# Kernel optimization log

Hardware: AMD Instinct MI355X
Metric: run time of the kernel (lower is better)

Reference implementation:

```python
import jax, jax.numpy as jnp
import numpy as np

N_RAYS = 131072
N_SAMPLES = 64
N_IMPORTANCE = 128
NEAR, FAR = 2.0, 6.0


def setup_inputs() -> dict:
    key = jax.random.key(0)
    k1, k2, k3, k4 = jax.random.split(key, 4)
    rays_o = jax.random.normal(k1, (N_RAYS, 3), dtype=jnp.float32)
    rays_d = jax.random.normal(k2, (N_RAYS, 3), dtype=jnp.float32)
    # z_vals must be monotonically increasing per ray (bin edges from coarse sampler)
    z_vals = jnp.sort(
        jax.random.uniform(k3, (N_RAYS, N_SAMPLES), dtype=jnp.float32,
                           minval=NEAR, maxval=FAR), axis=-1)
    weights = jax.random.uniform(k4, (N_RAYS, N_SAMPLES), dtype=jnp.float32)
    return {"rays_o": rays_o, "rays_d": rays_d, "z_vals": z_vals, "weights": weights}


def _sample_pdf(bins, weights):
    # bins: [N, B], weights: [N, B-1]; det=True since perturb == 0.0
    w = weights + 1e-5
    pdf = w / jnp.sum(w, axis=-1, keepdims=True)
    cdf = jnp.cumsum(pdf, axis=-1)
    cdf = jnp.concatenate([jnp.zeros_like(cdf[..., :1]), cdf], axis=-1)  # [N, B]
    u = jnp.linspace(0.0, 1.0, N_IMPORTANCE, dtype=cdf.dtype)
    u = jnp.broadcast_to(u, cdf.shape[:-1] + (N_IMPORTANCE,))  # [N, NI]
    # per-ray binary search (right=True)
    inds = jax.vmap(lambda c, uu: jnp.searchsorted(c, uu, side='right'))(cdf, u)
    below = jnp.maximum(inds - 1, 0)
    above = jnp.minimum(inds, cdf.shape[-1] - 1)
    cdf_b = jnp.take_along_axis(cdf, below, axis=-1)
    cdf_a = jnp.take_along_axis(cdf, above, axis=-1)
    bins_b = jnp.take_along_axis(bins, below, axis=-1)
    bins_a = jnp.take_along_axis(bins, above, axis=-1)
    denom = cdf_a - cdf_b
    denom = jnp.where(denom < 1e-5, jnp.ones_like(denom), denom)
    t = (u - cdf_b) / denom
    return bins_b + t * (bins_a - bins_b)  # [N, NI]


def reference(rays_o, rays_d, z_vals, weights):
    z_mid = 0.5 * (z_vals[..., 1:] + z_vals[..., :-1])          # [N, S-1]
    z_samples = _sample_pdf(z_mid, weights[..., 1:-1])           # [N, NI]
    z_samples = jax.lax.stop_gradient(z_samples)                 # .detach()
    z_all = jnp.sort(jnp.concatenate([z_vals, z_samples], -1), -1)  # [N, S+NI]
    pts = rays_o[:, None, :] + rays_d[:, None, :] * z_all[..., None]  # [N, S+NI, 3]
    return pts, z_all, z_samples
```

## Files before the change

### kernel.cpp

```cpp
#include <hip/hip_runtime.h>

#define NRAYS 131072
#define NS 64
#define NI 128
#define NM 63
#define NW 62
#define NT 192

__global__ __launch_bounds__(256) void importance_kernel(
    const float* __restrict__ rays_o,
    const float* __restrict__ rays_d,
    const float* __restrict__ z_vals,
    const float* __restrict__ weights,
    float* __restrict__ out_pts,
    float* __restrict__ out_zall,
    float* __restrict__ out_zs)
{
    __shared__ __align__(16) float s_zall[4][NT];

    const int wave = threadIdx.x >> 6;
    const int lane = threadIdx.x & 63;
    const int ray  = (blockIdx.x << 2) + wave;

    const float* zv_g = z_vals  + (size_t)ray * NS;
    const float* w_g  = weights + (size_t)ray * NS;

    const float zvl = zv_g[lane];
    const float wl  = (lane < NW) ? (w_g[lane + 1] + 1e-5f) : 0.0f;

    const int sray = __builtin_amdgcn_readfirstlane(ray);
    const float o0 = rays_o[3 * sray + 0], o1 = rays_o[3 * sray + 1], o2 = rays_o[3 * sray + 2];
    const float d0 = rays_d[3 * sray + 0], d1 = rays_d[3 * sray + 1], d2 = rays_d[3 * sray + 2];

    const float zm = 0.5f * (zvl + __shfl_down(zvl, 1, 64));

    float scan = wl;
    #pragma unroll
    for (int off = 1; off < 64; off <<= 1) {
        const float up = __shfl_up(scan, off, 64);
        if (lane >= off) scan += up;
    }
    const float total = __shfl(scan, NW - 1, 64);
    const float sp  = __shfl_up(scan, 1, 64);
    const float cdf = (lane == 0) ? 0.0f : sp / total;

    const float zm_m1  = __shfl_up(zm, 1, 64);
    const float cdf_m1 = __shfl_up(cdf, 1, 64);

    float U;
    {
        float rr = (zvl - zm_m1) / (zm - zm_m1);
        rr = fminf(fmaxf(rr, 0.0f), 1.0f);
        float dg = cdf - cdf_m1;
        if (dg < 1e-5f) dg = 1.0f;
        float uu = cdf_m1 + rr * dg;
        uu = fminf(uu, cdf);
        U = (lane == 0) ? 0.0f : ((lane == 63) ? 2.0f : uu);
    }

    int cnt;
    if (lane == 0) cnt = 0;
    else if (lane == 63) cnt = 128;
    else {
        const int g = (int)(U * 127.0f);
        int c = g - 1;
        #pragma unroll
        for (int t = -1; t <= 1; ++t) {
            const int j = g + t;
            bool lt;
            if (j < 0) lt = true;
            else if (j > 127) lt = false;
            else lt = ((float)((double)j * (1.0 / 127.0)) < U);
            c += lt ? 1 : 0;
        }
        cnt = c;
    }
    s_zall[wave][lane + cnt] = zvl;

    float xs0, xs1;
    #pragma unroll
    for (int rep = 0; rep < 2; rep++) {
        const int j = (lane << 1) + rep;
        const float u = (float)((double)j * (1.0 / 127.0));
        int lo = 0, hi = NM;
        #pragma unroll
        for (int it = 0; it < 6; it++) {
            const int mid = (lo + hi) >> 1;
            const float v = __shfl(cdf, mid, 64);
            if (lo < hi) { if (v <= u) lo = mid + 1; else hi = mid; }
        }
        const int below = lo - 1;
        const int above = (lo > NM - 1) ? (NM - 1) : lo;
        const float cb = __shfl(cdf, below, 64);
        const float ca = __shfl(cdf, above, 64);
        const float bb = __shfl(zm,  below, 64);
        const float ba = __shfl(zm,  above, 64);
        const float Ul = __shfl(U,   lo,    64);
        float denom = ca - cb;
        if (denom < 1e-5f) denom = 1.0f;
        const float t = (u - cb) / denom;
        const float x = bb + t * (ba - bb);
        const int pos = j + lo + ((Ul <= u) ? 1 : 0);
        s_zall[wave][pos] = x;
        if (rep == 0) xs0 = x; else xs1 = x;
    }

    asm volatile("s_waitcnt lgkmcnt(0)" ::: "memory");

    const float* zallp = s_zall[wave];

    const size_t pts_base = (size_t)ray * (NT * 3);
    #pragma unroll
    for (int rep = 0; rep < 3; rep++) {
        const int i4 = lane + (rep << 6);
        if (i4 < 144) {
            const int q  = i4 / 3;
            const int m  = i4 - 3 * q;
            const int k0 = i4 + q;
            const float za = zallp[k0];
            const float zb = zallp[k0 + 1];
            float4 v;
            #pragma unroll
            for (int t = 0; t < 4; t++) {
                const int mt = m + t;
                const float z  = (mt >= 3) ? zb : za;
                const int  ds  = (mt >= 3) ? (mt - 3) : mt;
                const float oo = (ds == 0) ? o0 : ((ds == 1) ? o1 : o2);
                const float dd = (ds == 0) ? d0 : ((ds == 1) ? d1 : d2);
                (&v.x)[t] = fmaf(dd, z, oo);
            }
            *reinterpret_cast<float4*>(out_pts + pts_base + ((size_t)i4 << 2)) = v;
        }
    }

    if (lane < 48) {
        const float4 v = *reinterpret_cast<const float4*>(&zallp[lane << 2]);
        *reinterpret_cast<float4*>(out_zall + (size_t)ray * NT + (lane << 2)) = v;
    }

    {
        float2 zz; zz.x = xs0; zz.y = xs1;
        *reinterpret_cast<float2*>(out_zs + (size_t)ray * NI + (lane << 1)) = zz;
    }
}

extern "C" void kernel_launch(void* const* d_in, const int* in_sizes, int n_in,
                              void* d_out, int out_size, void* d_ws, size_t ws_size,
                              hipStream_t stream) {
    const float* rays_o  = (const float*)d_in[0];
    const float* rays_d  = (const float*)d_in[1];
    const float* z_vals  = (const float*)d_in[2];
    const float* weights = (const float*)d_in[3];

    float* out      = (float*)d_out;
    float* out_pts  = out;
    float* out_zall = out + (size_t)NRAYS * NT * 3;
    float* out_zs   = out_zall + (size_t)NRAYS * NT;

    dim3 grid(NRAYS / 4), block(256);
    hipLaunchKernelGGL(importance_kernel, grid, block, 0, stream,
                       rays_o, rays_d, z_vals, weights,
                       out_pts, out_zall, out_zs);
}
```

Before: 515.2 us.

## Process eight rays per wave with next-ray input prefetch

Each wave now loops over eight consecutive rays instead of handling one, and the grid shrinks by the same factor. The next ray's z_vals and weights loads are issued before the current ray's compute, so global load latency can overlap the scan, search and store work. The aim is to cut block launch overhead and hide memory latency. The cost is fewer resident waves and a serial loop per wave, which may reduce overall parallelism and memory-level concurrency.

```diff
diff --git a/kernel.cpp b/kernel.cpp
--- a/kernel.cpp
+++ b/kernel.cpp
@@ -6,6 +6,7 @@
 #define NM 63
 #define NW 62
 #define NT 192
+#define RPW 8
 
 __global__ __launch_bounds__(256) void importance_kernel(
     const float* __restrict__ rays_o,
@@ -20,127 +21,141 @@
 
     const int wave = threadIdx.x >> 6;
     const int lane = threadIdx.x & 63;
-    const int ray  = (blockIdx.x << 2) + wave;
+    const int base = ((blockIdx.x << 2) + wave) * RPW;
 
-    const float* zv_g = z_vals  + (size_t)ray * NS;
-    const float* w_g  = weights + (size_t)ray * NS;
+    float* const zall_s = s_zall[wave];
 
-    const float zvl = zv_g[lane];
-    const float wl  = (lane < NW) ? (w_g[lane + 1] + 1e-5f) : 0.0f;
+    float zv_c = z_vals[(size_t)base * NS + lane];
+    float w_c  = (lane < NW) ? weights[(size_t)base * NS + 1 + lane] : 0.0f;
 
-    const int sray = __builtin_amdgcn_readfirstlane(ray);
-    const float o0 = rays_o[3 * sray + 0], o1 = rays_o[3 * sray + 1], o2 = rays_o[3 * sray + 2];
-    const float d0 = rays_d[3 * sray + 0], d1 = rays_d[3 * sray + 1], d2 = rays_d[3 * sray + 2];
+    #pragma unroll 1
+    for (int r = 0; r < RPW; ++r) {
+        const int ray = base + r;
 
-    const float zm = 0.5f * (zvl + __shfl_down(zvl, 1, 64));
+        float zv_n = 0.0f, w_n = 0.0f;
+        if (r + 1 < RPW) {
+            zv_n = z_vals[(size_t)(ray + 1) * NS + lane];
+            if (lane < NW) w_n = weights[(size_t)(ray + 1) * NS + 1 + lane];
+        }
 
-    float scan = wl;
-    #pragma unroll
-    for (int off = 1; off < 64; off <<= 1) {
-        const float up = __shfl_up(scan, off, 64);
-        if (lane >= off) scan += up;
-    }
-    const float total = __shfl(scan, NW - 1, 64);
-    const float sp  = __shfl_up(scan, 1, 64);
-    const float cdf = (lane == 0) ? 0.0f : sp / total;
+        const float zvl = zv_c;
+        const float wl  = (lane < NW) ? (w_c + 1e-5f) : 0.0f;
 
-    const float zm_m1  = __shfl_up(zm, 1, 64);
-    const float cdf_m1 = __shfl_up(cdf, 1, 64);
+        const int sray = __builtin_amdgcn_readfirstlane(ray);
+        const float o0 = rays_o[3 * sray + 0], o1 = rays_o[3 * sray + 1], o2 = rays_o[3 * sray + 2];
+        const float d0 = rays_d[3 * sray + 0], d1 = rays_d[3 * sray + 1], d2 = rays_d[3 * sray + 2];
 
-    float U;
-    {
-        float rr = (zvl - zm_m1) / (zm - zm_m1);
-        rr = fminf(fmaxf(rr, 0.0f), 1.0f);
-        float dg = cdf - cdf_m1;
-        if (dg < 1e-5f) dg = 1.0f;
-        float uu = cdf_m1 + rr * dg;
-        uu = fminf(uu, cdf);
-        U = (lane == 0) ? 0.0f : ((lane == 63) ? 2.0f : uu);
-    }
+        const float zm = 0.5f * (zvl + __shfl_down(zvl, 1, 64));
 
-    int cnt;
-    if (lane == 0) cnt = 0;
-    else if (lane == 63) cnt = 128;
-    else {
-        const int g = (int)(U * 127.0f);
-        int c = g - 1;
+        float scan = wl;
         #pragma unroll
-        for (int t = -1; t <= 1; ++t) {
-            const int j = g + t;
-            bool lt;
-            if (j < 0) lt = true;
-            else if (j > 127) lt = false;
-            else lt = ((float)((double)j * (1.0 / 127.0)) < U);
-            c += lt ? 1 : 0;
+        for (int off = 1; off < 64; off <<= 1) {
+            const float up = __shfl_up(scan, off, 64);
+            if (lane >= off) scan += up;
         }
-        cnt = c;
-    }
-    s_zall[wave][lane + cnt] = zvl;
+        const float total = __shfl(scan, NW - 1, 64);
+        const float sp  = __shfl_up(scan, 1, 64);
+        const float cdf = (lane == 0) ? 0.0f : sp / total;
 
-    float xs0, xs1;
-    #pragma unroll
-    for (int rep = 0; rep < 2; rep++) {
-        const int j = (lane << 1) + rep;
-        const float u = (float)((double)j * (1.0 / 127.0));
-        int lo = 0, hi = NM;
+        const float zm_m1  = __shfl_up(zm, 1, 64);
+        const float cdf_m1 = __shfl_up(cdf, 1, 64);
+
+        float U;
+        {
+            float rr = (zvl - zm_m1) / (zm - zm_m1);
+            rr = fminf(fmaxf(rr, 0.0f), 1.0f);
+            float dg = cdf - cdf_m1;
+            if (dg < 1e-5f) dg = 1.0f;
+            float uu = cdf_m1 + rr * dg;
+            uu = fminf(uu, cdf);
+            U = (lane == 0) ? 0.0f : ((lane == 63) ? 2.0f : uu);
+        }
+
+        int cnt;
+        if (lane == 0) cnt = 0;
+        else if (lane == 63) cnt = 128;
+        else {
+            const int g = (int)(U * 127.0f);
+            int c = g - 1;
+            #pragma unroll
+            for (int t = -1; t <= 1; ++t) {
+                const int j = g + t;
+                bool lt;
+                if (j < 0) lt = true;
+                else if (j > 127) lt = false;
+                else lt = ((float)((double)j * (1.0 / 127.0)) < U);
+                c += lt ? 1 : 0;
+            }
+            cnt = c;
+        }
+        zall_s[lane + cnt] = zvl;
+
+        float xs0, xs1;
         #pragma unroll
-        for (int it = 0; it < 6; it++) {
-            const int mid = (lo + hi) >> 1;
-            const float v = __shfl(cdf, mid, 64);
-            if (lo < hi) { if (v <= u) lo = mid + 1; else hi = mid; }
+        for (int rep = 0; rep < 2; rep++) {
+            const int j = (lane << 1) + rep;
+            const float u = (float)((double)j * (1.0 / 127.0));
+            int lo = 0, hi = NM;
+            #pragma unroll
+            for (int it = 0; it < 6; it++) {
+                const int mid = (lo + hi) >> 1;
+                const float v = __shfl(cdf, mid, 64);
+                if (lo < hi) { if (v <= u) lo = mid + 1; else hi = mid; }
+            }
+            const int below = lo - 1;
+            const int above = (lo > NM - 1) ? (NM - 1) : lo;
+            const float cb = __shfl(cdf, below, 64);
+            const float ca = __shfl(cdf, above, 64);
+            const float bb = __shfl(zm,  below, 64);
+            const float ba = __shfl(zm,  above, 64);
+            const float Ul = __shfl(U,   lo,    64);
+            float denom = ca - cb;
+            if (denom < 1e-5f) denom = 1.0f;
+            const float t = (u - cb) / denom;
+            const float x = bb + t * (ba - bb);
+            const int pos = j + lo + ((Ul <= u) ? 1 : 0);
+            zall_s[pos] = x;
+            if (rep == 0) xs0 = x; else xs1 = x;
         }
-        const int below = lo - 1;
-        const int above = (lo > NM - 1) ? (NM - 1) : lo;
-        const float cb = __shfl(cdf, below, 64);
-        const float ca = __shfl(cdf, above, 64);
-        const float bb = __shfl(zm,  below, 64);
-        const float ba = __shfl(zm,  above, 64);
-        const float Ul = __shfl(U,   lo,    64);
-        float denom = ca - cb;
-        if (denom < 1e-5f) denom = 1.0f;
-        const float t = (u - cb) / denom;
-        const float x = bb + t * (ba - bb);
-        const int pos = j + lo + ((Ul <= u) ? 1 : 0);
-        s_zall[wave][pos] = x;
-        if (rep == 0) xs0 = x; else xs1 = x;
-    }
 
-    asm volatile("s_waitcnt lgkmcnt(0)" ::: "memory");
+        {
+            float2 zz; zz.x = xs0; zz.y = xs1;
+            *reinterpret_cast<float2*>(out_zs + (size_t)ray * NI + (lane << 1)) = zz;
+        }
 
-    const float* zallp = s_zall[wave];
+        asm volatile("s_waitcnt lgkmcnt(0)" ::: "memory");
 
-    const size_t pts_base = (size_t)ray * (NT * 3);
-    #pragma unroll
-    for (int rep = 0; rep < 3; rep++) {
-        const int i4 = lane + (rep << 6);
-        if (i4 < 144) {
-            const int q  = i4 / 3;
-            const int m  = i4 - 3 * q;
-            const int k0 = i4 + q;
-            const float za = zallp[k0];
-            const float zb = zallp[k0 + 1];
-            float4 v;
-            #pragma unroll
-            for (int t = 0; t < 4; t++) {
-                const int mt = m + t;
-                const float z  = (mt >= 3) ? zb : za;
-                const int  ds  = (mt >= 3) ? (mt - 3) : mt;
-                const float oo = (ds == 0) ? o0 : ((ds == 1) ? o1 : o2);
-                const float dd = (ds == 0) ? d0 : ((ds == 1) ? d1 : d2);
-                (&v.x)[t] = fmaf(dd, z, oo);
+        const size_t pts_base = (size_t)ray * (NT * 3);
+        #pragma unroll
+        for (int rep = 0; rep < 3; rep++) {
+            const int i4 = lane + (rep << 6);
+            if (i4 < 144) {
+                const int q  = i4 / 3;
+                const int m  = i4 - 3 * q;
+                const int k0 = i4 + q;
+                const float za = zall_s[k0];
+                const float zb = zall_s[k0 + 1];
+                float4 v;
+                #pragma unroll
+                for (int t = 0; t < 4; t++) {
+                    const int mt = m + t;
+                    const float z  = (mt >= 3) ? zb : za;
+                    const int  ds  = (mt >= 3) ? (mt - 3) : mt;
+                    const float oo = (ds == 0) ? o0 : ((ds == 1) ? o1 : o2);
+                    const float dd = (ds == 0) ? d0 : ((ds == 1) ? d1 : d2);
+                    (&v.x)[t] = fmaf(dd, z, oo);
+                }
+                *reinterpret_cast<float4*>(out_pts + pts_base + ((size_t)i4 << 2)) = v;
             }
-            *reinterpret_cast<float4*>(out_pts + pts_base + ((size_t)i4 << 2)) = v;
         }
-    }
 
-    if (lane < 48) {
-        const float4 v = *reinterpret_cast<const float4*>(&zallp[lane << 2]);
-        *reinterpret_cast<float4*>(out_zall + (size_t)ray * NT + (lane << 2)) = v;
-    }
+        if (lane < 48) {
+            const float4 v = *reinterpret_cast<const float4*>(&zall_s[lane << 2]);
+            *reinterpret_cast<float4*>(out_zall + (size_t)ray * NT + (lane << 2)) = v;
+        }
 
-    {
-        float2 zz; zz.x = xs0; zz.y = xs1;
-        *reinterpret_cast<float2*>(out_zs + (size_t)ray * NI + (lane << 1)) = zz;
+        zv_c = zv_n;
+        w_c  = w_n;
     }
 }
 
@@ -157,7 +172,7 @@
     float* out_zall = out + (size_t)NRAYS * NT * 3;
     float* out_zs   = out_zall + (size_t)NRAYS * NT;
 
-    dim3 grid(NRAYS / 4), block(256);
+    dim3 grid(NRAYS / (4 * RPW)), block(256);
     hipLaunchKernelGGL(importance_kernel, grid, block, 0, stream,
                        rays_o, rays_d, z_vals, weights,
                        out_pts, out_zall, out_zs);
```

Measured after the change: 534.7 us. +3.8%, slower.

## Split fused kernel into sampling and point-generation kernels via global z_all

Applied to the files above, without the earlier changes.

The single kernel is split in two. The first computes the importance samples and scatters z_all straight to global memory instead of staging it in LDS. The second reads z_all back from global memory and writes the 3D points. This removes LDS use and may ease register pressure in each kernel, but it adds a second launch, a global-memory round trip for z_all, and uncoalesced scattered global stores.

```diff
diff --git a/kernel.cpp b/kernel.cpp
--- a/kernel.cpp
+++ b/kernel.cpp
@@ -7,30 +7,19 @@
 #define NW 62
 #define NT 192
 
-__global__ __launch_bounds__(256) void importance_kernel(
-    const float* __restrict__ rays_o,
-    const float* __restrict__ rays_d,
+__global__ __launch_bounds__(256, 4) void sample_kernel(
     const float* __restrict__ z_vals,
     const float* __restrict__ weights,
-    float* __restrict__ out_pts,
     float* __restrict__ out_zall,
     float* __restrict__ out_zs)
 {
-    __shared__ __align__(16) float s_zall[4][NT];
-
     const int wave = threadIdx.x >> 6;
     const int lane = threadIdx.x & 63;
     const int ray  = (blockIdx.x << 2) + wave;
 
-    const float* zv_g = z_vals  + (size_t)ray * NS;
-    const float* w_g  = weights + (size_t)ray * NS;
-
-    const float zvl = zv_g[lane];
-    const float wl  = (lane < NW) ? (w_g[lane + 1] + 1e-5f) : 0.0f;
-
-    const int sray = __builtin_amdgcn_readfirstlane(ray);
-    const float o0 = rays_o[3 * sray + 0], o1 = rays_o[3 * sray + 1], o2 = rays_o[3 * sray + 2];
-    const float d0 = rays_d[3 * sray + 0], d1 = rays_d[3 * sray + 1], d2 = rays_d[3 * sray + 2];
+    const float zvl = z_vals[(size_t)ray * NS + lane];
+    const float wl  = (lane < NW) ? (weights[(size_t)ray * NS + 1 + lane] + 1e-5f)
+                                  : 0.0f;
 
     const float zm = 0.5f * (zvl + __shfl_down(zvl, 1, 64));
 
@@ -58,6 +47,8 @@
         U = (lane == 0) ? 0.0f : ((lane == 63) ? 2.0f : uu);
     }
 
+    const size_t za_base = (size_t)ray * NT;
+
     int cnt;
     if (lane == 0) cnt = 0;
     else if (lane == 63) cnt = 128;
@@ -75,7 +66,7 @@
         }
         cnt = c;
     }
-    s_zall[wave][lane + cnt] = zvl;
+    out_zall[za_base + lane + cnt] = zvl;
 
     float xs0, xs1;
     #pragma unroll
@@ -101,15 +92,31 @@
         const float t = (u - cb) / denom;
         const float x = bb + t * (ba - bb);
         const int pos = j + lo + ((Ul <= u) ? 1 : 0);
-        s_zall[wave][pos] = x;
+        out_zall[za_base + pos] = x;
         if (rep == 0) xs0 = x; else xs1 = x;
     }
 
-    asm volatile("s_waitcnt lgkmcnt(0)" ::: "memory");
+    float2 zz; zz.x = xs0; zz.y = xs1;
+    *reinterpret_cast<float2*>(out_zs + (size_t)ray * NI + (lane << 1)) = zz;
+}
 
-    const float* zallp = s_zall[wave];
+__global__ __launch_bounds__(256) void pts_kernel(
+    const float* __restrict__ rays_o,
+    const float* __restrict__ rays_d,
+    const float* __restrict__ zall,
+    float* __restrict__ out_pts)
+{
+    const int wave = threadIdx.x >> 6;
+    const int lane = threadIdx.x & 63;
+    const int ray  = (blockIdx.x << 2) + wave;
 
+    const int sray = __builtin_amdgcn_readfirstlane(ray);
+    const float o0 = rays_o[3 * sray + 0], o1 = rays_o[3 * sray + 1], o2 = rays_o[3 * sray + 2];
+    const float d0 = rays_d[3 * sray + 0], d1 = rays_d[3 * sray + 1], d2 = rays_d[3 * sray + 2];
+
+    const float* zp = zall + (size_t)ray * NT;
     const size_t pts_base = (size_t)ray * (NT * 3);
+
     #pragma unroll
     for (int rep = 0; rep < 3; rep++) {
         const int i4 = lane + (rep << 6);
@@ -117,8 +124,8 @@
             const int q  = i4 / 3;
             const int m  = i4 - 3 * q;
             const int k0 = i4 + q;
-            const float za = zallp[k0];
-            const float zb = zallp[k0 + 1];
+            const float za = zp[k0];
+            const float zb = zp[k0 + 1];
             float4 v;
             #pragma unroll
             for (int t = 0; t < 4; t++) {
@@ -131,16 +138,6 @@
             }
             *reinterpret_cast<float4*>(out_pts + pts_base + ((size_t)i4 << 2)) = v;
         }
-    }
-
-    if (lane < 48) {
-        const float4 v = *reinterpret_cast<const float4*>(&zallp[lane << 2]);
-        *reinterpret_cast<float4*>(out_zall + (size_t)ray * NT + (lane << 2)) = v;
-    }
-
-    {
-        float2 zz; zz.x = xs0; zz.y = xs1;
-        *reinterpret_cast<float2*>(out_zs + (size_t)ray * NI + (lane << 1)) = zz;
     }
 }
 
@@ -158,7 +155,8 @@
     float* out_zs   = out_zall + (size_t)NRAYS * NT;
 
     dim3 grid(NRAYS / 4), block(256);
-    hipLaunchKernelGGL(importance_kernel, grid, block, 0, stream,
-                       rays_o, rays_d, z_vals, weights,
-                       out_pts, out_zall, out_zs);
+    hipLaunchKernelGGL(sample_kernel, grid, block, 0, stream,
+                       z_vals, weights, out_zall, out_zs);
+    hipLaunchKernelGGL(pts_kernel, grid, block, 0, stream,
+                       rays_o, rays_d, out_zall, out_pts);
 }
```

Result: slower. 543.2 us (+5.4%).
